# Kernel tuning notes

Hardware: AMD Instinct MI355X
Metric: run time of the kernel (lower is better)

The kernel has to match this reference:

```python
import jax, jax.numpy as jnp
import numpy as np

B, S, D_MODEL, D_K, D_V = 8, 2048, 1024, 1024, 1024


def setup_inputs() -> dict:
    key = jax.random.key(0)
    ks = jax.random.split(key, 10)
    scale = 1.0 / np.sqrt(D_MODEL)
    return {
        "inputs_q": jax.random.normal(ks[0], (B, S, D_MODEL), dtype=jnp.float32),
        "inputs_k": jax.random.normal(ks[1], (B, S, D_MODEL), dtype=jnp.float32),
        "inputs_v": jax.random.normal(ks[2], (B, S, D_MODEL), dtype=jnp.float32),
        "mask": jax.random.randint(ks[3], (B, S), 0, 2, dtype=jnp.int32),
        "Wq": jax.random.normal(ks[4], (D_MODEL, D_K), dtype=jnp.float32) * scale,
        "bq": jnp.zeros((D_K,), dtype=jnp.float32),
        "Wk": jax.random.normal(ks[5], (D_MODEL, D_K), dtype=jnp.float32) * scale,
        "bk": jnp.zeros((D_K,), dtype=jnp.float32),
        "Wv": jax.random.normal(ks[6], (D_MODEL, D_V), dtype=jnp.float32) * scale,
        "bv": jnp.zeros((D_V,), dtype=jnp.float32),
    }


def reference(inputs_q, inputs_k, inputs_v, mask, Wq, bq, Wk, bk, Wv, bv):
    # Dense projections: [B,S,d_model] @ [d_model,d] + bias
    q = jnp.einsum("bsd,dk->bsk", inputs_q, Wq) + bq
    k = jnp.einsum("bsd,dk->bsk", inputs_k, Wk) + bk
    v = jnp.einsum("bsd,dv->bsv", inputs_v, Wv) + bv
    # scaled dot-product scores [B,S,S]
    scores = jnp.einsum("bqk,bsk->bqs", q, k) / jnp.sqrt(jnp.float32(D_K))
    # padding mask [B,S] -> matrix mask via min(row, col); 1 = valid
    m = mask.astype(jnp.float32)
    matrix_mask = jnp.minimum(m[:, :, None], m[:, None, :])  # [B,S,S]
    mask_float = 1.0 - matrix_mask  # 1 where masked
    scores = scores + mask_float * (-1e9)
    attention_weights = jax.nn.softmax(scores, axis=-1)
    out = jnp.einsum("bqs,bsv->bqv", attention_weights, v)  # [B,S,d_v]
    return out
```

## Files before the change

kernel.cpp:

```cpp
#include <hip/hip_runtime.h>
#include <stdint.h>


typedef unsigned short u16;
typedef __attribute__((ext_vector_type(8))) short short8;
typedef __attribute__((ext_vector_type(4))) float f32x4;

__device__ __forceinline__ u16 f2bf(float x) {
  unsigned u = __float_as_uint(x);
  return (u16)((u + 0x7FFFu + ((u >> 16) & 1u)) >> 16);
}
__device__ __forceinline__ float bf2f(u16 h) {
  return __uint_as_float(((unsigned)h) << 16);
}

__device__ __forceinline__ void stage16(const void* g, void* l) {
  const __attribute__((address_space(1))) uint32_t* gp =
      (const __attribute__((address_space(1))) uint32_t*)(uintptr_t)g;
  __attribute__((address_space(3))) uint32_t* lp =
      (__attribute__((address_space(3))) uint32_t*)(uintptr_t)l;
  __builtin_amdgcn_global_load_lds(gp, lp, 16, 0, 0);
}

__device__ __forceinline__ short8 ld8(const char* p, int off) {
  return *(const short8*)(p + off);
}

__global__ __launch_bounds__(256) void maskscan(const int* __restrict__ mask,
                                                int* __restrict__ idxA,
                                                int* __restrict__ nvA,
                                                int* __restrict__ nvpadA,
                                                int* __restrict__ nvp128A) {
  const int b = blockIdx.x;
  const int t = threadIdx.x, lane = t & 63, w = t >> 6;
  const int* m = mask + b * 2048;
  int v[8], loc = 0;
#pragma unroll
  for (int i = 0; i < 8; ++i) { v[i] = m[t * 8 + i]; loc += v[i]; }
  int sc = loc;
  for (int off = 1; off < 64; off <<= 1) {
    int n = __shfl_up(sc, off);
    if (lane >= off) sc += n;
  }
  __shared__ int wsum[4];
  if (lane == 63) wsum[w] = sc;
  __syncthreads();
  int woff = 0;
  for (int i = 0; i < w; ++i) woff += wsum[i];
  int pos = woff + sc - loc;
#pragma unroll
  for (int i = 0; i < 8; ++i)
    if (v[i]) idxA[b * 2048 + (pos++)] = t * 8 + i;
  if (t == 255) {
    const int nv = woff + sc;
    nvA[b] = nv;
    nvpadA[b] = (nv + 255) & ~255;
    nvp128A[b] = (nv + 127) & ~127;
  }
}

__global__ __launch_bounds__(256) void compact3(const float* __restrict__ Xq,
                                                const float* __restrict__ Xk,
                                                const float* __restrict__ Xv,
                                                const int* __restrict__ idxA,
                                                const int* __restrict__ nvA,
                                                u16* __restrict__ Oq,
                                                u16* __restrict__ Ok,
                                                u16* __restrict__ Ov) {
  const int b = blockIdx.y, j = blockIdx.x, z = blockIdx.z;
  if (j >= nvA[b]) return;
  const float* X = (z == 0) ? Xq : (z == 1) ? Xk : Xv;
  u16* out = (z == 0) ? Oq : (z == 1) ? Ok : Ov;
  const int src = idxA[b * 2048 + j];
  const float4* s = (const float4*)(X + ((size_t)b * 2048 + src) * 1024);
  ushort4* d = (ushort4*)(out + ((size_t)b * 2048 + j) * 1024);
  const float4 f = s[threadIdx.x];
  ushort4 o;
  o.x = f2bf(f.x); o.y = f2bf(f.y); o.z = f2bf(f.z); o.w = f2bf(f.w);
  d[threadIdx.x] = o;
}

__global__ __launch_bounds__(256) void colpart(const float* __restrict__ X,
                                               float* __restrict__ partial) {
  const int b = blockIdx.x, dq = blockIdx.y, sck = blockIdx.z;
  const int d = dq * 256 + threadIdx.x;
  const float* p = X + ((size_t)b * 2048 + sck * 256) * 1024 + d;
  float s0 = 0, s1 = 0, s2 = 0, s3 = 0;
  for (int r = 0; r < 256; r += 4) {
    s0 += p[(size_t)(r + 0) * 1024];
    s1 += p[(size_t)(r + 1) * 1024];
    s2 += p[(size_t)(r + 2) * 1024];
    s3 += p[(size_t)(r + 3) * 1024];
  }
  partial[((size_t)b * 8 + sck) * 1024 + d] = (s0 + s1) + (s2 + s3);
}

__global__ __launch_bounds__(256) void vpartk(const float* __restrict__ partial,
                                              const float* __restrict__ Wv,
                                              float* __restrict__ vpart) {
  const int b = blockIdx.x, cq = blockIdx.y, dk = blockIdx.z;
  const int t = threadIdx.x;
  __shared__ float mx[128];
  if (t < 128) {
    const int d = dk * 128 + t;
    float m = 0;
#pragma unroll
    for (int i = 0; i < 8; ++i) m += partial[((size_t)b * 8 + i) * 1024 + d];
    mx[t] = m * (1.0f / 2048.0f);
  }
  __syncthreads();
  const int c = cq * 256 + t;
  const float* wp = Wv + (size_t)(dk * 128) * 1024 + c;
  float acc = 0;
#pragma unroll 4
  for (int i = 0; i < 128; ++i) acc += mx[i] * wp[(size_t)i * 1024];
  vpart[((size_t)b * 8 + dk) * 1024 + c] = acc;
}

__global__ __launch_bounds__(256) void vmeanred(const float* __restrict__ vpart,
                                                const float* __restrict__ bv,
                                                float* __restrict__ vmean) {
  const int b = blockIdx.x;
  const int c = blockIdx.y * 256 + threadIdx.x;
  float acc = bv[c];
#pragma unroll
  for (int i = 0; i < 8; ++i) acc += vpart[((size_t)b * 8 + i) * 1024 + c];
  vmean[b * 1024 + c] = acc;
}

__global__ __launch_bounds__(256) void bcast(const int* __restrict__ mask,
                                             const float* __restrict__ vmean,
                                             float* __restrict__ out) {
  const int b = blockIdx.y, row = blockIdx.x;
  if (mask[b * 2048 + row] != 0) return;
  const float4 vv = ((const float4*)(vmean + b * 1024))[threadIdx.x];
  ((float4*)(out + ((size_t)b * 2048 + row) * 1024))[threadIdx.x] = vv;
}

__global__ __launch_bounds__(256) void wtrans3(const float* __restrict__ Wq,
                                               const float* __restrict__ Wk,
                                               const float* __restrict__ Wv,
                                               u16* __restrict__ WT) {
  __shared__ float tile[32][33];
  const int z = blockIdx.z;
  const float* W = (z == 0) ? Wq : (z == 1) ? Wk : Wv;
  u16* out = WT + (size_t)z * 1024 * 1024;
  const int tx = threadIdx.x, ty = threadIdx.y;
  const int d0 = blockIdx.y * 32, n0 = blockIdx.x * 32;
#pragma unroll
  for (int i = 0; i < 4; ++i)
    tile[ty + 8 * i][tx] = W[(size_t)(d0 + ty + 8 * i) * 1024 + n0 + tx];
  __syncthreads();
#pragma unroll
  for (int i = 0; i < 4; ++i)
    out[(size_t)(n0 + ty + 8 * i) * 1024 + d0 + tx] = f2bf(tile[tx][ty + 8 * i]);
}

#define BAR __builtin_amdgcn_s_barrier()
#define SB __builtin_amdgcn_sched_barrier(0)
#define LGK0 asm volatile("s_waitcnt lgkmcnt(0)" ::: "memory")
#define VM4 asm volatile("s_waitcnt vmcnt(4)" ::: "memory")
#define VM0 asm volatile("s_waitcnt vmcnt(0)" ::: "memory")

#define RDA4(P0, P1, MH)                                      \
  {                                                           \
    _Pragma("unroll") for (int mf_ = 0; mf_ < 4; ++mf_) {     \
      afr[0][mf_] = ld8(P0, (MH) * 8192 + mf_ * 2048);        \
      afr[1][mf_] = ld8(P1, (MH) * 8192 + mf_ * 2048);        \
    }                                                         \
  }

#define RDB2(DST, P0, P1, NH)                                 \
  {                                                           \
    DST[0][0] = ld8(P0, (NH) * 4096);                         \
    DST[0][1] = ld8(P0, (NH) * 4096 + 2048);                  \
    DST[1][0] = ld8(P1, (NH) * 4096);                         \
    DST[1][1] = ld8(P1, (NH) * 4096 + 2048);                  \
  }

#define MQ16(ACC, NH, BF)                                                \
  __builtin_amdgcn_s_setprio(1);                                         \
  {                                                                      \
    _Pragma("unroll") for (int ks_ = 0; ks_ < 2; ++ks_)                  \
        _Pragma("unroll") for (int mf_ = 0; mf_ < 4; ++mf_)              \
            _Pragma("unroll") for (int nf_ = 0; nf_ < 2; ++nf_)          \
                ACC[mf_][(NH) * 2 + nf_] =                               \
                    __builtin_amdgcn_mfma_f32_16x16x32_bf16(             \
                        afr[ks_][mf_], BF[ks_][nf_],                     \
                        ACC[mf_][(NH) * 2 + nf_], 0, 0, 0);              \
  }                                                                      \
  __builtin_amdgcn_s_setprio(0);

template <int MODE>
__global__ __launch_bounds__(512, 2) void gemm8p(
    const u16* __restrict__ A, const u16* __restrict__ B,
    void* __restrict__ C, void* __restrict__ C1, void* __restrict__ C2,
    const float* __restrict__ b0, const float* __restrict__ b1,
    const float* __restrict__ b2,
    const int* __restrict__ nvpadA,
    int K, int lda, int ldb, int ldc) {
  __shared__ __attribute__((aligned(16))) char smem[131072];
  const int tid = threadIdx.x;
  const int lane = tid & 63;
  const int w = tid >> 6;
  const int wr = w >> 2;
  const int wc = w & 3;

  const int bx = blockIdx.x;
  const int z = bx & 7;
  int r = bx >> 3;
  const int o = r >> 5; r &= 31;
  const int bm = r >> 2, bn = r & 3;

  const int nvp = nvpadA[z];
  if (bm * 256 >= nvp) return;

  const u16* Ap = A + (size_t)o * (8u * 2048u * 1024u) + (size_t)z * (2048u * 1024u);
  const u16* Bp = B + (size_t)o * (1024u * 1024u);
  const int half = K >> 7;

  const int srow = w * 8 + (lane >> 3);
  const int scol = ((lane & 7) ^ (lane >> 3)) << 3;
  const u16* Ab0 = Ap + (size_t)(bm * 256 + srow) * lda + scol;
  const u16* Ab1 = Ab0 + (size_t)64 * lda;
  const u16* Ab2 = Ab0 + (size_t)128 * lda;
  const u16* Ab3 = Ab0 + (size_t)192 * lda;
  const u16* Bb0 = Bp + (size_t)(bn * 256 + srow) * ldb + scol;
  const u16* Bb1 = Bb0 + (size_t)64 * ldb;
  const u16* Bb2 = Bb0 + (size_t)128 * ldb;
  const u16* Bb3 = Bb0 + (size_t)192 * ldb;
  char* ldsW = smem + w * 1024;

  const int fr = lane & 15;
  const int fq = lane >> 4;
  const int fx = (fr & 7) << 4;
  const char* pak0 = smem + wr * 16384 + fr * 128 + ((fq * 16) ^ fx);
  const char* pak1 = smem + wr * 16384 + fr * 128 + ((64 + fq * 16) ^ fx);
  const char* pak0b = pak0 + 65536;
  const char* pak1b = pak1 + 65536;
  const char* pbk0 = smem + 32768 + wc * 8192 + fr * 128 + ((fq * 16) ^ fx);
  const char* pbk1 = smem + 32768 + wc * 8192 + fr * 128 + ((64 + fq * 16) ^ fx);
  const char* pbk0b = pbk0 + 65536;
  const char* pbk1b = pbk1 + 65536;

  f32x4 acc0[4][4] = {};
  f32x4 acc1[4][4] = {};
  short8 afr[2][4], bf0[2][2], bf1[2][2];

  stage16(Bb0, ldsW + 32768); stage16(Bb1, ldsW + 40960);
  stage16(Bb2, ldsW + 49152); stage16(Bb3, ldsW + 57344);
  stage16(Ab0, ldsW + 0);     stage16(Ab1, ldsW + 8192);
  stage16(Ab2, ldsW + 16384); stage16(Ab3, ldsW + 24576);
  stage16(Bb0 + 64, ldsW + 98304);  stage16(Bb1 + 64, ldsW + 106496);
  stage16(Bb2 + 64, ldsW + 114688); stage16(Bb3 + 64, ldsW + 122880);
  VM4;
  BAR;

  int koff = 0;
  for (int i = 0; i < half - 1; ++i) {
    const int o1 = koff + 64, o2 = koff + 128, o3 = koff + 192;
    RDA4(pak0, pak1, 0); RDB2(bf0, pbk0, pbk1, 0);
    stage16(Ab0 + o1, ldsW + 65536); stage16(Ab1 + o1, ldsW + 73728);
    SB; BAR; LGK0; MQ16(acc0, 0, bf0); BAR;
    RDB2(bf1, pbk0, pbk1, 1);
    stage16(Ab2 + o1, ldsW + 81920); stage16(Ab3 + o1, ldsW + 90112);
    SB; BAR; LGK0; MQ16(acc0, 1, bf1); BAR;
    RDA4(pak0, pak1, 1);
    stage16(Bb0 + o2, ldsW + 32768); stage16(Bb1 + o2, ldsW + 40960);
    SB; BAR; LGK0; MQ16(acc1, 0, bf0); BAR;
    stage16(Bb2 + o2, ldsW + 49152); stage16(Bb3 + o2, ldsW + 57344);
    SB; BAR; MQ16(acc1, 1, bf1); VM4; BAR;
    RDA4(pak0b, pak1b, 0); RDB2(bf0, pbk0b, pbk1b, 0);
    stage16(Ab0 + o2, ldsW + 0); stage16(Ab1 + o2, ldsW + 8192);
    SB; BAR; LGK0; MQ16(acc0, 0, bf0); BAR;
    RDB2(bf1, pbk0b, pbk1b, 1);
    stage16(Ab2 + o2, ldsW + 16384); stage16(Ab3 + o2, ldsW + 24576);
    SB; BAR; LGK0; MQ16(acc0, 1, bf1); BAR;
    RDA4(pak0b, pak1b, 1);
    stage16(Bb0 + o3, ldsW + 98304); stage16(Bb1 + o3, ldsW + 106496);
    SB; BAR; LGK0; MQ16(acc1, 0, bf0); BAR;
    stage16(Bb2 + o3, ldsW + 114688); stage16(Bb3 + o3, ldsW + 122880);
    SB; BAR; MQ16(acc1, 1, bf1); VM4; BAR;
    koff += 128;
  }
  {
    const int o1 = koff + 64;
    RDA4(pak0, pak1, 0); RDB2(bf0, pbk0, pbk1, 0);
    stage16(Ab0 + o1, ldsW + 65536); stage16(Ab1 + o1, ldsW + 73728);
    SB; BAR; LGK0; MQ16(acc0, 0, bf0); BAR;
    RDB2(bf1, pbk0, pbk1, 1);
    stage16(Ab2 + o1, ldsW + 81920); stage16(Ab3 + o1, ldsW + 90112);
    SB; BAR; LGK0; MQ16(acc0, 1, bf1); BAR;
    RDA4(pak0, pak1, 1);
    SB; BAR; LGK0; MQ16(acc1, 0, bf0); BAR;
    SB; BAR; MQ16(acc1, 1, bf1); VM0; BAR;
    RDA4(pak0b, pak1b, 0); RDB2(bf0, pbk0b, pbk1b, 0);
    SB; BAR; LGK0; MQ16(acc0, 0, bf0); BAR;
    RDB2(bf1, pbk0b, pbk1b, 1);
    SB; BAR; LGK0; MQ16(acc0, 1, bf1); BAR;
    RDA4(pak0b, pak1b, 1);
    SB; BAR; LGK0; MQ16(acc1, 0, bf0); BAR;
    SB; BAR; MQ16(acc1, 1, bf1); BAR;
  }

  const int colb = bn * 256 + wc * 64 + fr;
#pragma unroll
  for (int mh = 0; mh < 2; ++mh) {
    f32x4(&ac)[4][4] = mh ? acc1 : acc0;
    const int rowl = bm * 256 + wr * 128 + mh * 64 + fq * 4;
    if (o < 2) {
      const float* bp = o ? b1 : b0;
      u16* Cb = (u16*)(o ? C1 : C) + (size_t)z * (2048u * 1024u);
#pragma unroll
      for (int mf = 0; mf < 4; ++mf)
#pragma unroll
        for (int n = 0; n < 4; ++n) {
          const int c = colb + n * 16;
          const float bv = bp[c];
#pragma unroll
          for (int j = 0; j < 4; ++j)
            Cb[(size_t)(rowl + mf * 16 + j) * ldc + c] = f2bf(ac[mf][n][j] + bv);
        }
    } else {
      u16* Cb = (u16*)C2;
#pragma unroll
      for (int mf = 0; mf < 4; ++mf) {
        const int s_ = rowl + mf * 16;
#pragma unroll
        for (int n = 0; n < 4; ++n) {
          const int c = colb + n * 16;
          const float bv = b2[c];
          ushort4 ov;
          ov.x = f2bf(ac[mf][n][0] + bv);
          ov.y = f2bf(ac[mf][n][1] + bv);
          ov.z = f2bf(ac[mf][n][2] + bv);
          ov.w = f2bf(ac[mf][n][3] + bv);
          *(ushort4*)&Cb[((size_t)z * 1024 + c) * 2048 + s_] = ov;
        }
      }
    }
  }
}

template <int MODE>
__global__ __launch_bounds__(256, 2) void gemm128(
    const u16* __restrict__ A, const u16* __restrict__ B, void* __restrict__ C,
    const int* __restrict__ nvp128A, const int* __restrict__ nvA,
    const int* __restrict__ idxA,
    int K, int lda, int ldb, int ldc,
    size_t Az, size_t Bz, size_t Cz) {
  __shared__ __attribute__((aligned(16))) u16 lsA[128 * 32];
  __shared__ __attribute__((aligned(16))) u16 lsB[128 * 32];
  const int tid = threadIdx.x;
  const int lane = tid & 63;
  const int w = tid >> 6;
  const int wr = w >> 1, wc = w & 1;

  const int bx = blockIdx.x;
  const int z = bx & 7;
  const int r = bx >> 3;
  int bm, bn;
  if constexpr (MODE == 2) { bm = r >> 4; bn = r & 15; }
  else                     { bm = r >> 3; bn = r & 7; }

  const int nvp = nvp128A[z];
  if (bm * 128 >= nvp) return;
  if constexpr (MODE == 2) { if (bn * 128 >= nvp) return; }
  const int Kz = (MODE == 3) ? nvp : K;

  const u16* Ap = A + (size_t)z * Az;
  const u16* Bp = B + (size_t)z * Bz;

  const int srow = lane >> 2;
  const int scol = (lane & 3) * 8;
  const u16* Ag0 = Ap + (size_t)(bm * 128 + w * 32 + srow) * lda + scol;
  const u16* Ag1 = Ag0 + (size_t)16 * lda;
  const u16* Bg0 = Bp + (size_t)(bn * 128 + w * 32 + srow) * ldb + scol;
  const u16* Bg1 = Bg0 + (size_t)16 * ldb;
  u16* lA0 = &lsA[(w * 32) * 32];
  u16* lA1 = &lsA[(w * 32 + 16) * 32];
  u16* lB0 = &lsB[(w * 32) * 32];
  u16* lB1 = &lsB[(w * 32 + 16) * 32];

  const int arow = wr * 64 + (lane & 15);
  const int brow = wc * 64 + (lane & 15);
  const int ko = (lane >> 4) * 8;

  f32x4 acc[4][4] = {};

  for (int k0 = 0; k0 < Kz; k0 += 32) {
    stage16(Ag0 + k0, lA0);
    stage16(Ag1 + k0, lA1);
    stage16(Bg0 + k0, lB0);
    stage16(Bg1 + k0, lB1);
    __syncthreads();
    short8 af[4], bfr[4];
#pragma unroll
    for (int m = 0; m < 4; ++m)
      af[m] = *(const short8*)&lsA[(arow + m * 16) * 32 + ko];
#pragma unroll
    for (int n = 0; n < 4; ++n)
      bfr[n] = *(const short8*)&lsB[(brow + n * 16) * 32 + ko];
#pragma unroll
    for (int m = 0; m < 4; ++m)
#pragma unroll
      for (int n = 0; n < 4; ++n)
        acc[m][n] =
            __builtin_amdgcn_mfma_f32_16x16x32_bf16(af[m], bfr[n], acc[m][n], 0, 0, 0);
    __syncthreads();
  }

  const int col0 = bn * 128 + wc * 64 + (lane & 15);
  const int row0 = bm * 128 + wr * 64 + ((lane >> 4) << 2);

  if constexpr (MODE == 2) {
    u16* Cb = (u16*)C + (size_t)z * Cz;
#pragma unroll
    for (int m = 0; m < 4; ++m)
#pragma unroll
      for (int n = 0; n < 4; ++n) {
        const int c = col0 + n * 16;
#pragma unroll
        for (int j = 0; j < 4; ++j)
          Cb[(size_t)(row0 + m * 16 + j) * ldc + c] =
              f2bf(acc[m][n][j] * 0.03125f);
      }
  } else {
    const int nv = nvA[z];
    const int* idxp = idxA + z * 2048;
    float* Ob = (float*)C;
#pragma unroll
    for (int m = 0; m < 4; ++m)
#pragma unroll
      for (int j = 0; j < 4; ++j) {
        const int rowc = row0 + m * 16 + j;
        if (rowc < nv) {
          const int gr = idxp[rowc];
          float* orow = Ob + ((size_t)z * 2048 + gr) * 1024;
#pragma unroll
          for (int n = 0; n < 4; ++n) orow[col0 + n * 16] = acc[m][n][j];
        }
      }
  }
}

__global__ __launch_bounds__(256) void softmaxc(u16* __restrict__ scores,
                                                const int* __restrict__ nvA,
                                                const int* __restrict__ nvp128A) {
  const int b = blockIdx.y, row = blockIdx.x;
  const int nv = nvA[b];
  if (row >= nv) return;
  const int nvp = nvp128A[b];
  const int t = threadIdx.x, lane = t & 63, w = t >> 6;
  u16* sc = scores + ((size_t)b * 2048 + row) * 2048;
  const int c0 = t * 8;
  float v[8];
  if (c0 < nvp) {
    const ushort4 h0 = *(const ushort4*)&sc[c0];
    const ushort4 h1 = *(const ushort4*)&sc[c0 + 4];
    v[0] = bf2f(h0.x); v[1] = bf2f(h0.y); v[2] = bf2f(h0.z); v[3] = bf2f(h0.w);
    v[4] = bf2f(h1.x); v[5] = bf2f(h1.y); v[6] = bf2f(h1.z); v[7] = bf2f(h1.w);
  } else {
#pragma unroll
    for (int i = 0; i < 8; ++i) v[i] = 0.f;
  }
  float lmax = -3.0e38f;
#pragma unroll
  for (int i = 0; i < 8; ++i)
    if (c0 + i < nv) lmax = fmaxf(lmax, v[i]);
#pragma unroll
  for (int off = 32; off >= 1; off >>= 1) lmax = fmaxf(lmax, __shfl_xor(lmax, off));
  __shared__ float red[8];
  if (lane == 0) red[w] = lmax;
  __syncthreads();
  const float bmax = fmaxf(fmaxf(red[0], red[1]), fmaxf(red[2], red[3]));
  float e[8];
  float lsum = 0.f;
#pragma unroll
  for (int i = 0; i < 8; ++i) {
    e[i] = (c0 + i < nv) ? __expf(v[i] - bmax) : 0.f;
    lsum += e[i];
  }
#pragma unroll
  for (int off = 32; off >= 1; off >>= 1) lsum += __shfl_xor(lsum, off);
  if (lane == 0) red[4 + w] = lsum;
  __syncthreads();
  const float inv = 1.0f / ((red[4] + red[5]) + (red[6] + red[7]));
  if (c0 < nvp) {
    ushort4 o0, o1;
    o0.x = f2bf(e[0] * inv); o0.y = f2bf(e[1] * inv);
    o0.z = f2bf(e[2] * inv); o0.w = f2bf(e[3] * inv);
    o1.x = f2bf(e[4] * inv); o1.y = f2bf(e[5] * inv);
    o1.z = f2bf(e[6] * inv); o1.w = f2bf(e[7] * inv);
    *(ushort4*)&sc[c0] = o0;
    *(ushort4*)&sc[c0 + 4] = o1;
  }
}

extern "C" void kernel_launch(void* const* d_in, const int* in_sizes, int n_in,
                              void* d_out, int out_size, void* d_ws, size_t ws_size,
                              hipStream_t stream) {
  const float* in_q = (const float*)d_in[0];
  const float* in_k = (const float*)d_in[1];
  const float* in_v = (const float*)d_in[2];
  const int* mask = (const int*)d_in[3];
  const float* Wq = (const float*)d_in[4];
  const float* bq = (const float*)d_in[5];
  const float* Wk = (const float*)d_in[6];
  const float* bk = (const float*)d_in[7];
  const float* Wv = (const float*)d_in[8];
  const float* bv = (const float*)d_in[9];

  char* ws = (char*)d_ws;
  const size_t SZ = (size_t)16384 * 1024 * 2;
  u16* qc = (u16*)(ws);
  u16* kc = (u16*)(ws + SZ);
  u16* vcT = (u16*)(ws + 2 * SZ);
  u16* Xc = (u16*)(ws + 3 * SZ);
  u16* Xqc = Xc;
  u16* Xkc = Xc + (size_t)8 * 2048 * 1024;
  u16* Xvc = Xkc + (size_t)8 * 2048 * 1024;
  u16* scores = (u16*)(ws + 3 * SZ);
  u16* WT = (u16*)(ws + 6 * SZ);
  char* misc = ws + 6 * SZ + 6 * 1024 * 1024;
  int* idxA = (int*)misc;
  int* nvA = idxA + 8 * 2048;
  int* nvpadA = nvA + 8;
  int* nvp128A = nvpadA + 8;
  float* partial = (float*)(misc + 128 * 1024);
  float* vmean = (float*)(misc + 384 * 1024);
  float* vpart = (float*)(misc + 448 * 1024);

  maskscan<<<8, 256, 0, stream>>>(mask, idxA, nvA, nvpadA, nvp128A);

  compact3<<<dim3(2048, 8, 3), 256, 0, stream>>>(in_q, in_k, in_v, idxA, nvA,
                                                 Xqc, Xkc, Xvc);
  colpart<<<dim3(8, 4, 8), 256, 0, stream>>>(in_v, partial);
  vpartk<<<dim3(8, 4, 8), 256, 0, stream>>>(partial, Wv, vpart);
  vmeanred<<<dim3(8, 4), 256, 0, stream>>>(vpart, bv, vmean);

  wtrans3<<<dim3(32, 32, 3), dim3(32, 8), 0, stream>>>(Wq, Wk, Wv, WT);

  gemm8p<0><<<768, 512, 0, stream>>>(
      Xqc, WT, qc, kc, vcT, bq, bk, bv, nvpadA, 1024, 1024, 1024, 1024);

  gemm128<2><<<2048, 256, 0, stream>>>(
      qc, kc, scores, nvp128A, nvA, idxA, 1024, 1024, 1024, 2048,
      (size_t)2048 * 1024, (size_t)2048 * 1024, (size_t)2048 * 2048);

  softmaxc<<<dim3(2048, 8), 256, 0, stream>>>(scores, nvA, nvp128A);

  gemm128<3><<<1024, 256, 0, stream>>>(
      scores, vcT, d_out, nvp128A, nvA, idxA, 0, 2048, 2048, 1024,
      (size_t)2048 * 2048, (size_t)1024 * 2048, 0);

  bcast<<<dim3(2048, 8), 256, 0, stream>>>(mask, vmean, (float*)d_out);
}
```

Before: 255.7 us.

## Double-buffer gemm128 LDS staging and fuse weight transpose with column sums

gemm128 now uses two LDS buffers. The next K-tile is issued with global_load_lds while MFMAs run on the current tile, which halves the barriers per iteration and lets loads overlap compute. The weight transpose and the V column-sum partial kernels are merged into one launch indexed by a flat block id, removing a kernel launch. The 256-row padded count is dropped and gemm8p's early exit now uses the 128-padded count, which skips the same blocks. In exchange, gemm128 uses twice the LDS per block, which may lower occupancy.

```diff
diff --git a/kernel.cpp b/kernel.cpp
--- a/kernel.cpp
+++ b/kernel.cpp
@@ -29,7 +29,6 @@
 __global__ __launch_bounds__(256) void maskscan(const int* __restrict__ mask,
                                                 int* __restrict__ idxA,
                                                 int* __restrict__ nvA,
-                                                int* __restrict__ nvpadA,
                                                 int* __restrict__ nvp128A) {
   const int b = blockIdx.x;
   const int t = threadIdx.x, lane = t & 63, w = t >> 6;
@@ -54,7 +53,6 @@
   if (t == 255) {
     const int nv = woff + sc;
     nvA[b] = nv;
-    nvpadA[b] = (nv + 255) & ~255;
     nvp128A[b] = (nv + 127) & ~127;
   }
 }
@@ -80,19 +78,43 @@
   d[threadIdx.x] = o;
 }
 
-__global__ __launch_bounds__(256) void colpart(const float* __restrict__ X,
-                                               float* __restrict__ partial) {
-  const int b = blockIdx.x, dq = blockIdx.y, sck = blockIdx.z;
-  const int d = dq * 256 + threadIdx.x;
-  const float* p = X + ((size_t)b * 2048 + sck * 256) * 1024 + d;
-  float s0 = 0, s1 = 0, s2 = 0, s3 = 0;
-  for (int r = 0; r < 256; r += 4) {
-    s0 += p[(size_t)(r + 0) * 1024];
-    s1 += p[(size_t)(r + 1) * 1024];
-    s2 += p[(size_t)(r + 2) * 1024];
-    s3 += p[(size_t)(r + 3) * 1024];
-  }
-  partial[((size_t)b * 8 + sck) * 1024 + d] = (s0 + s1) + (s2 + s3);
+__global__ __launch_bounds__(256) void wtcol(const float* __restrict__ Wq,
+                                             const float* __restrict__ Wk,
+                                             const float* __restrict__ Wv,
+                                             u16* __restrict__ WT,
+                                             const float* __restrict__ Xv,
+                                             float* __restrict__ partial) {
+  const int bid = blockIdx.x;
+  const int t = threadIdx.x;
+  if (bid < 3072) {
+    __shared__ float tile[32][33];
+    const int z = bid >> 10;
+    const int xy = bid & 1023;
+    const int n0 = (xy & 31) * 32, d0 = (xy >> 5) * 32;
+    const float* W = (z == 0) ? Wq : (z == 1) ? Wk : Wv;
+    u16* out = WT + (size_t)z * 1024 * 1024;
+    const int tx = t & 31, ty = t >> 5;
+#pragma unroll
+    for (int i = 0; i < 4; ++i)
+      tile[ty + 8 * i][tx] = W[(size_t)(d0 + ty + 8 * i) * 1024 + n0 + tx];
+    __syncthreads();
+#pragma unroll
+    for (int i = 0; i < 4; ++i)
+      out[(size_t)(n0 + ty + 8 * i) * 1024 + d0 + tx] = f2bf(tile[tx][ty + 8 * i]);
+  } else {
+    const int r = bid - 3072;
+    const int b = r & 7, dq = (r >> 3) & 3, sck = r >> 5;
+    const int d = dq * 256 + t;
+    const float* p = Xv + ((size_t)b * 2048 + sck * 256) * 1024 + d;
+    float s0 = 0, s1 = 0, s2 = 0, s3 = 0;
+    for (int rr = 0; rr < 256; rr += 4) {
+      s0 += p[(size_t)(rr + 0) * 1024];
+      s1 += p[(size_t)(rr + 1) * 1024];
+      s2 += p[(size_t)(rr + 2) * 1024];
+      s3 += p[(size_t)(rr + 3) * 1024];
+    }
+    partial[((size_t)b * 8 + sck) * 1024 + d] = (s0 + s1) + (s2 + s3);
+  }
 }
 
 __global__ __launch_bounds__(256) void vpartk(const float* __restrict__ partial,
@@ -135,25 +157,6 @@
   if (mask[b * 2048 + row] != 0) return;
   const float4 vv = ((const float4*)(vmean + b * 1024))[threadIdx.x];
   ((float4*)(out + ((size_t)b * 2048 + row) * 1024))[threadIdx.x] = vv;
-}
-
-__global__ __launch_bounds__(256) void wtrans3(const float* __restrict__ Wq,
-                                               const float* __restrict__ Wk,
-                                               const float* __restrict__ Wv,
-                                               u16* __restrict__ WT) {
-  __shared__ float tile[32][33];
-  const int z = blockIdx.z;
-  const float* W = (z == 0) ? Wq : (z == 1) ? Wk : Wv;
-  u16* out = WT + (size_t)z * 1024 * 1024;
-  const int tx = threadIdx.x, ty = threadIdx.y;
-  const int d0 = blockIdx.y * 32, n0 = blockIdx.x * 32;
-#pragma unroll
-  for (int i = 0; i < 4; ++i)
-    tile[ty + 8 * i][tx] = W[(size_t)(d0 + ty + 8 * i) * 1024 + n0 + tx];
-  __syncthreads();
-#pragma unroll
-  for (int i = 0; i < 4; ++i)
-    out[(size_t)(n0 + ty + 8 * i) * 1024 + d0 + tx] = f2bf(tile[tx][ty + 8 * i]);
 }
 
 #define BAR __builtin_amdgcn_s_barrier()
@@ -191,13 +194,12 @@
   }                                                                      \
   __builtin_amdgcn_s_setprio(0);
 
-template <int MODE>
 __global__ __launch_bounds__(512, 2) void gemm8p(
     const u16* __restrict__ A, const u16* __restrict__ B,
     void* __restrict__ C, void* __restrict__ C1, void* __restrict__ C2,
     const float* __restrict__ b0, const float* __restrict__ b1,
     const float* __restrict__ b2,
-    const int* __restrict__ nvpadA,
+    const int* __restrict__ nvp128A,
     int K, int lda, int ldb, int ldc) {
   __shared__ __attribute__((aligned(16))) char smem[131072];
   const int tid = threadIdx.x;
@@ -212,7 +214,7 @@
   const int o = r >> 5; r &= 31;
   const int bm = r >> 2, bn = r & 3;
 
-  const int nvp = nvpadA[z];
+  const int nvp = nvp128A[z];
   if (bm * 256 >= nvp) return;
 
   const u16* Ap = A + (size_t)o * (8u * 2048u * 1024u) + (size_t)z * (2048u * 1024u);
@@ -349,8 +351,8 @@
     const int* __restrict__ idxA,
     int K, int lda, int ldb, int ldc,
     size_t Az, size_t Bz, size_t Cz) {
-  __shared__ __attribute__((aligned(16))) u16 lsA[128 * 32];
-  __shared__ __attribute__((aligned(16))) u16 lsB[128 * 32];
+  __shared__ __attribute__((aligned(16))) u16 lsA[2 * 128 * 32];
+  __shared__ __attribute__((aligned(16))) u16 lsB[2 * 128 * 32];
   const int tid = threadIdx.x;
   const int lane = tid & 63;
   const int w = tid >> 6;
@@ -388,27 +390,44 @@
 
   f32x4 acc[4][4] = {};
 
-  for (int k0 = 0; k0 < Kz; k0 += 32) {
-    stage16(Ag0 + k0, lA0);
-    stage16(Ag1 + k0, lA1);
-    stage16(Bg0 + k0, lB0);
-    stage16(Bg1 + k0, lB1);
-    __syncthreads();
+  auto compute = [&](int cur) {
+    const u16* sA = lsA + cur * 4096;
+    const u16* sB = lsB + cur * 4096;
     short8 af[4], bfr[4];
 #pragma unroll
     for (int m = 0; m < 4; ++m)
-      af[m] = *(const short8*)&lsA[(arow + m * 16) * 32 + ko];
+      af[m] = *(const short8*)&sA[(arow + m * 16) * 32 + ko];
 #pragma unroll
     for (int n = 0; n < 4; ++n)
-      bfr[n] = *(const short8*)&lsB[(brow + n * 16) * 32 + ko];
+      bfr[n] = *(const short8*)&sB[(brow + n * 16) * 32 + ko];
 #pragma unroll
     for (int m = 0; m < 4; ++m)
 #pragma unroll
       for (int n = 0; n < 4; ++n)
         acc[m][n] =
             __builtin_amdgcn_mfma_f32_16x16x32_bf16(af[m], bfr[n], acc[m][n], 0, 0, 0);
+  };
+
+  stage16(Ag0, lA0);
+  stage16(Ag1, lA1);
+  stage16(Bg0, lB0);
+  stage16(Bg1, lB1);
+  __syncthreads();
+
+  int cur = 0;
+  int k0 = 0;
+  for (; k0 + 32 < Kz; k0 += 32) {
+    const int off = (cur ^ 1) * 4096;
+    const int kn = k0 + 32;
+    stage16(Ag0 + kn, lA0 + off);
+    stage16(Ag1 + kn, lA1 + off);
+    stage16(Bg0 + kn, lB0 + off);
+    stage16(Bg1 + kn, lB1 + off);
+    compute(cur);
     __syncthreads();
-  }
+    cur ^= 1;
+  }
+  compute(cur);
 
   const int col0 = bn * 128 + wc * 64 + (lane & 15);
   const int row0 = bm * 128 + wr * 64 + ((lane >> 4) << 2);
@@ -525,24 +544,21 @@
   char* misc = ws + 6 * SZ + 6 * 1024 * 1024;
   int* idxA = (int*)misc;
   int* nvA = idxA + 8 * 2048;
-  int* nvpadA = nvA + 8;
-  int* nvp128A = nvpadA + 8;
+  int* nvp128A = nvA + 8;
   float* partial = (float*)(misc + 128 * 1024);
   float* vmean = (float*)(misc + 384 * 1024);
   float* vpart = (float*)(misc + 448 * 1024);
 
-  maskscan<<<8, 256, 0, stream>>>(mask, idxA, nvA, nvpadA, nvp128A);
+  maskscan<<<8, 256, 0, stream>>>(mask, idxA, nvA, nvp128A);
 
   compact3<<<dim3(2048, 8, 3), 256, 0, stream>>>(in_q, in_k, in_v, idxA, nvA,
                                                  Xqc, Xkc, Xvc);
-  colpart<<<dim3(8, 4, 8), 256, 0, stream>>>(in_v, partial);
+  wtcol<<<3328, 256, 0, stream>>>(Wq, Wk, Wv, WT, in_v, partial);
   vpartk<<<dim3(8, 4, 8), 256, 0, stream>>>(partial, Wv, vpart);
   vmeanred<<<dim3(8, 4), 256, 0, stream>>>(vpart, bv, vmean);
 
-  wtrans3<<<dim3(32, 32, 3), dim3(32, 8), 0, stream>>>(Wq, Wk, Wv, WT);
-
-  gemm8p<0><<<768, 512, 0, stream>>>(
-      Xqc, WT, qc, kc, vcT, bq, bk, bv, nvpadA, 1024, 1024, 1024, 1024);
+  gemm8p<<<768, 512, 0, stream>>>(
+      Xqc, WT, qc, kc, vcT, bq, bk, bv, nvp128A, 1024, 1024, 1024, 1024);
 
   gemm128<2><<<2048, 256, 0, stream>>>(
       qc, kc, scores, nvp128A, nvA, idxA, 1024, 1024, 1024, 2048,
```

After: 252.3 us. No clear change (-1.3%).
